# Kernel tuning notes

Hardware: AMD Instinct MI355X
Metric: run time of the kernel (lower is better)

The kernel has to match this reference:

```python
import jax, jax.numpy as jnp
import numpy as np

N0, N1, N2 = 512, 2048, 8192   # targets, hop1, hop2 node counts
K = 33                          # nneighbor + self loop
IN, HID, OUT, NH = 256, 128, 128, 8
NEG = -9.0e15
ALPHA = 0.2                     # LeakyReLU negative slope


def setup_inputs() -> dict:
    key = jax.random.key(0)
    ks = jax.random.split(key, 8)
    feats = jax.random.normal(ks[0], (N2, IN), jnp.float32)
    # xavier-ish scaled params (gain 1.414)
    W1 = jax.random.normal(ks[1], (NH, IN, HID), jnp.float32) * 0.072
    a1 = jax.random.normal(ks[2], (NH, 2 * HID), jnp.float32) * 0.105
    W2 = jax.random.normal(ks[3], (HID * NH, OUT), jnp.float32) * 0.042
    a2 = jax.random.normal(ks[4], (2 * OUT,), jnp.float32) * 0.105
    # layer1 edges: each of N1 targets gets K distinct neighbors in [0, N2)
    tgt1 = jnp.repeat(jnp.arange(N1, dtype=jnp.int32), K)
    dst1 = ((jnp.arange(N1)[:, None] * 97 + jnp.arange(K)[None, :] * 131) % N2).astype(jnp.int32).reshape(-1)
    src1 = jax.random.randint(ks[5], (N1 * K,), 0, N2, jnp.int32)
    # layer2 edges: each of N0 targets gets K distinct neighbors in [0, N1)
    tgt2 = jnp.repeat(jnp.arange(N0, dtype=jnp.int32), K)
    dst2 = ((jnp.arange(N0)[:, None] * 53 + jnp.arange(K)[None, :] * 61) % N1).astype(jnp.int32).reshape(-1)
    src2 = jax.random.randint(ks[6], (N0 * K,), 0, N1, jnp.int32)
    return dict(feats=feats, W1=W1, a1=a1, W2=W2, a2=a2,
                src1=src1, dst1=dst1, tgt1=tgt1, src2=src2, dst2=dst2, tgt2=tgt2)


def gat_layer(x, W, a, src, dst, tgt, t_len):
    # x: [n, in], W: [in, d], a: [2d]
    h = x @ W                                   # [n, d]
    d = h.shape[1]
    # concat([h[src], h[dst]]) @ a  ==  h[src]@a[:d] + h[dst]@a[d:]
    e = h[src] @ a[:d] + h[dst] @ a[d:]         # [E]
    e = jnp.where(e > 0, e, ALPHA * e)          # LeakyReLU
    att = jnp.full((t_len, h.shape[0]), NEG, h.dtype).at[tgt, dst].set(e)
    att = jax.nn.softmax(att, axis=1)           # dense row softmax (masked entries ~0)
    return jax.nn.elu(att @ h)                  # [t_len, d]


def reference(feats, W1, a1, W2, a2, src1, dst1, tgt1, src2, dst2, tgt2):
    # layer 1: nhead independent GAT heads over hop2 features
    heads = jax.vmap(lambda W, a: gat_layer(feats, W, a, src1, dst1, tgt1, N1))(W1, a1)  # [NH, N1, HID]
    x = jnp.transpose(heads, (1, 0, 2)).reshape(N1, NH * HID)  # torch.cat(dim=1)
    # layer 2: single GAT layer producing [N0, OUT]
    return gat_layer(x, W2, a2, src2, dst2, tgt2, N0)
```

## Files before the change

kernel.cpp:

```cpp
#include <hip/hip_runtime.h>
#include <math.h>

#define ALPHA 0.2f

constexpr int CN0 = 512, CN1 = 2048, CN2 = 8192, CK = 33;
constexpr int CIN = 256, CHID = 128, CNH = 8;

using u16    = unsigned short;
using f32x4  = __attribute__((ext_vector_type(4))) float;
using bf16x8 = __attribute__((ext_vector_type(8))) short;
using short8 = __attribute__((ext_vector_type(8))) short;

__device__ __forceinline__ u16 f2bf(float f) {
    unsigned u = __float_as_uint(f);
    u += 0x7fff + ((u >> 16) & 1);
    return (u16)(u >> 16);
}
__device__ __forceinline__ float bf2f(u16 h) {
    return __uint_as_float(((unsigned)h) << 16);
}

#define GLD16(g, l)                                                        \
    __builtin_amdgcn_global_load_lds(                                      \
        (const __attribute__((address_space(1))) void*)(g),                \
        (__attribute__((address_space(3))) void*)(l), 16, 0, 0)

__global__ __launch_bounds__(256) void prep_k(const float* __restrict__ feats,
                                              u16* __restrict__ fb,
                                              const float* __restrict__ W1,
                                              u16* __restrict__ w1t,
                                              const float* __restrict__ W2,
                                              u16* __restrict__ w2t,
                                              const float* __restrict__ a1,
                                              float* __restrict__ pvec) {
    __shared__ float t[32][33];
    int b = blockIdx.x;
    if (b < 2048) {
        const int i = (b * 256 + threadIdx.x) * 4;
        const float4 v = *reinterpret_cast<const float4*>(feats + i);
        *reinterpret_cast<ushort4*>(fb + i) =
            make_ushort4(f2bf(v.x), f2bf(v.y), f2bf(v.z), f2bf(v.w));
        return;
    }
    if (b >= 2432) {
        const int i = b - 2432;
        const int h = i >> 1, half = i & 1;
        const int j = threadIdx.x;
        const float* wrow = W1 + (size_t)h * CIN * CHID + (size_t)j * CHID;
        const float* ah   = a1 + h * 2 * CHID + half * CHID;
        float d = 0.f;
#pragma unroll 8
        for (int c = 0; c < CHID; ++c) d = fmaf(wrow[c], ah[c], d);
        pvec[(h * 2 + half) * CIN + j] = d;
        return;
    }
    b -= 2048;
    const float* ip;
    u16* op;
    int R, C, r0, c0;
    if (b < 256) {
        const int h = b >> 5, w = b & 31;
        ip = W1 + (size_t)h * CIN * CHID;
        op = w1t + (size_t)h * CIN * CHID;
        R = CIN; C = CHID; r0 = (w >> 2) * 32; c0 = (w & 3) * 32;
    } else {
        b -= 256;
        ip = W2; op = w2t;
        R = CNH * CHID; C = CHID; r0 = (b >> 2) * 32; c0 = (b & 3) * 32;
    }
    const int tx = threadIdx.x & 31, ty = threadIdx.x >> 5;
#pragma unroll
    for (int i = 0; i < 4; ++i)
        t[ty + 8 * i][tx] = ip[(size_t)(r0 + ty + 8 * i) * C + c0 + tx];
    __syncthreads();
#pragma unroll
    for (int i = 0; i < 4; ++i)
        op[(size_t)(c0 + ty + 8 * i) * R + r0 + tx] = f2bf(t[tx][ty + 8 * i]);
}

__global__ __launch_bounds__(256) void sgemm1_k(const u16* __restrict__ fb,
                                                const float* __restrict__ pvec,
                                                float* __restrict__ s1,
                                                float* __restrict__ s2) {
    const int node = (blockIdx.x * 256 + threadIdx.x) >> 6;
    const int lane = threadIdx.x & 63;
    const ushort4 hv = *reinterpret_cast<const ushort4*>(fb + (size_t)node * CIN + lane * 4);
    const float v0 = bf2f(hv.x), v1 = bf2f(hv.y), v2 = bf2f(hv.z), v3 = bf2f(hv.w);
#pragma unroll
    for (int h = 0; h < CNH; ++h) {
        const float4 p1 = *reinterpret_cast<const float4*>(pvec + (h * 2 + 0) * CIN + lane * 4);
        const float4 p2 = *reinterpret_cast<const float4*>(pvec + (h * 2 + 1) * CIN + lane * 4);
        float d1 = v0 * p1.x + v1 * p1.y + v2 * p1.z + v3 * p1.w;
        float d2 = v0 * p2.x + v1 * p2.y + v2 * p2.z + v3 * p2.w;
#pragma unroll
        for (int m = 1; m < 64; m <<= 1) {
            d1 += __shfl_xor(d1, m);
            d2 += __shfl_xor(d2, m);
        }
        if (lane == 0) {
            s1[h * CN2 + node] = d1;
            s2[h * CN2 + node] = d2;
        }
    }
}

__global__ __launch_bounds__(128) void agg1g_k(const float* __restrict__ s1,
                                               const float* __restrict__ s2,
                                               const int* __restrict__ src,
                                               const int* __restrict__ dst,
                                               const u16* __restrict__ fb,
                                               u16* __restrict__ gb) {
    __shared__ float wgt[CNH][CK];
    __shared__ int dsts[CK];

    const int t    = blockIdx.x;
    const int tid  = threadIdx.x;
    const int wv   = tid >> 6;
    const int lane = tid & 63;

    int sv = 0, dv = 0;
    if (lane < CK) {
        sv = src[t * CK + lane];
        dv = dst[t * CK + lane];
        if (tid < CK) dsts[tid] = dv;
    }
#pragma unroll
    for (int hh = 0; hh < 4; ++hh) {
        const int head = wv * 4 + hh;
        float e = -3.0e38f;
        if (lane < CK) {
            const float ee = s1[head * CN2 + sv] + s2[head * CN2 + dv];
            e = (ee > 0.f) ? ee : ALPHA * ee;
        }
        float m = e;
#pragma unroll
        for (int mm = 1; mm < 64; mm <<= 1) m = fmaxf(m, __shfl_xor(m, mm));
        const float p = (lane < CK) ? __expf(e - m) : 0.f;
        float s = p;
#pragma unroll
        for (int mm = 1; mm < 64; mm <<= 1) s += __shfl_xor(s, mm);
        if (lane < CK) wgt[head][lane] = p / s;
    }
    __syncthreads();

    const int c2 = tid * 2;
    float acc[CNH][2];
#pragma unroll
    for (int h = 0; h < CNH; ++h) { acc[h][0] = 0.f; acc[h][1] = 0.f; }
#pragma unroll 4
    for (int k = 0; k < CK; ++k) {
        const unsigned w2 = *reinterpret_cast<const unsigned*>(
            fb + (size_t)dsts[k] * CIN + c2);
        const float f0 = bf2f((u16)(w2 & 0xffff));
        const float f1 = bf2f((u16)(w2 >> 16));
#pragma unroll
        for (int h = 0; h < CNH; ++h) {
            const float wk = wgt[h][k];
            acc[h][0] = fmaf(wk, f0, acc[h][0]);
            acc[h][1] = fmaf(wk, f1, acc[h][1]);
        }
    }
#pragma unroll
    for (int h = 0; h < CNH; ++h) {
        const unsigned o = ((unsigned)f2bf(acc[h][1]) << 16) | f2bf(acc[h][0]);
        *reinterpret_cast<unsigned*>(gb + ((size_t)h * CN1 + t) * CIN + c2) = o;
    }
}

template <int KSTEPS, bool BF16OUT, bool ELUOUT, bool HEADSPLIT>
__global__ __launch_bounds__(256) void gemm_mfma(const u16* __restrict__ A, int lda,
                                                 const u16* __restrict__ Bt, int ldb,
                                                 u16* __restrict__ Cb,
                                                 float* __restrict__ Cf, int ldc,
                                                 long csplit) {
    constexpr int SMEMSZ = BF16OUT ? (128 * 136 * 2) : 32768;
    __shared__ __attribute__((aligned(16))) char smem[SMEMSZ];

    const int tid  = threadIdx.x;
    const int lane = tid & 63;
    const int wave = tid >> 6;
    const int row0 = blockIdx.y * 128;

    int kbase, bcol0, ccol0;
    if constexpr (HEADSPLIT) {
        A  += (size_t)blockIdx.z * CN1 * CIN;
        Bt += (size_t)blockIdx.z * CHID * CIN;
        kbase = 0; bcol0 = 0; ccol0 = blockIdx.z * CHID;
    } else {
        kbase = blockIdx.z * (KSTEPS * 32);
        bcol0 = blockIdx.x * 128;
        ccol0 = bcol0;
    }
    const int wr = (wave >> 1) * 64;
    const int wc = (wave & 1) * 64;

    f32x4 acc[4][4];
#pragma unroll
    for (int m = 0; m < 4; ++m)
#pragma unroll
        for (int n = 0; n < 4; ++n) acc[m][n] = (f32x4){0.f, 0.f, 0.f, 0.f};

    const int r0c = tid >> 2;
    const int cs0 = tid & 3;
    const int c0  = (cs0 - (r0c >> 1)) & 3;
    const int r1c = r0c + 64;

    const u16* ga0 = A + (size_t)(row0 + r0c) * lda + kbase + c0 * 8;
    const u16* ga1 = A + (size_t)(row0 + r1c) * lda + kbase + c0 * 8;
    const u16* gb0 = Bt + (size_t)(bcol0 + r0c) * ldb + kbase + c0 * 8;
    const u16* gb1 = Bt + (size_t)(bcol0 + r1c) * ldb + kbase + c0 * 8;

    auto STAGE = [&](int s) {
        const int k0 = s * 32;
        char* base = smem + (s & 1) * 16384;
        u16* as = (u16*)base + wave * 512;
        u16* bs = (u16*)(base + 8192) + wave * 512;
        GLD16(ga0 + k0, as);
        GLD16(ga1 + k0, as + 2048);
        GLD16(gb0 + k0, bs);
        GLD16(gb1 + k0, bs + 2048);
    };

    STAGE(0);
    __syncthreads();

    for (int s = 0; s < KSTEPS; ++s) {
        if (s + 1 < KSTEPS) STAGE(s + 1);

        const u16* Acur = (const u16*)(smem + (s & 1) * 16384);
        const u16* Bcur = Acur + 4096;

        bf16x8 af[4], bfr[4];
#pragma unroll
        for (int m = 0; m < 4; ++m) {
            const int rt = wr + m * 16 + (lane & 15);
            const int cs = ((lane >> 4) + (rt >> 1)) & 3;
            af[m] = *reinterpret_cast<const bf16x8*>(Acur + rt * 32 + cs * 8);
            const int rt2 = wc + m * 16 + (lane & 15);
            const int cs2 = ((lane >> 4) + (rt2 >> 1)) & 3;
            bfr[m] = *reinterpret_cast<const bf16x8*>(Bcur + rt2 * 32 + cs2 * 8);
        }
#pragma unroll
        for (int m = 0; m < 4; ++m)
#pragma unroll
            for (int n = 0; n < 4; ++n)
                acc[m][n] = __builtin_amdgcn_mfma_f32_16x16x32_bf16(
                    af[m], bfr[n], acc[m][n], 0, 0, 0);

        __syncthreads();
    }

    if constexpr (BF16OUT) {
        u16* Cs = (u16*)smem;
#pragma unroll
        for (int m = 0; m < 4; ++m) {
            const int rr = wr + m * 16 + (lane >> 4) * 4;
#pragma unroll
            for (int n = 0; n < 4; ++n) {
                const int cc = wc + n * 16 + (lane & 15);
#pragma unroll
                for (int q = 0; q < 4; ++q) {
                    float v = acc[m][n][q];
                    if (ELUOUT) v = (v > 0.f) ? v : __expf(v) - 1.f;
                    Cs[(rr + q) * 136 + cc] = f2bf(v);
                }
            }
        }
        __syncthreads();
#pragma unroll
        for (int i = 0; i < 8; ++i) {
            const int cid = i * 256 + tid;
            const int r  = cid >> 4;
            const int kc = cid & 15;
            const int4 v = *reinterpret_cast<const int4*>(&Cs[r * 136 + kc * 8]);
            *reinterpret_cast<int4*>(&Cb[(long)(row0 + r) * ldc + ccol0 + kc * 8]) = v;
        }
    } else {
        const long cbase = HEADSPLIT ? 0 : (long)blockIdx.z * csplit;
#pragma unroll
        for (int m = 0; m < 4; ++m) {
            const int rr = row0 + wr + m * 16 + (lane >> 4) * 4;
#pragma unroll
            for (int n = 0; n < 4; ++n) {
                const int cc = ccol0 + wc + n * 16 + (lane & 15);
#pragma unroll
                for (int q = 0; q < 4; ++q)
                    Cf[cbase + (long)(rr + q) * ldc + cc] = acc[m][n][q];
            }
        }
    }
}

__global__ __launch_bounds__(256) void scores2_k(const float* __restrict__ part,
                                                 const float* __restrict__ a,
                                                 float* __restrict__ h2,
                                                 float* __restrict__ s1,
                                                 float* __restrict__ s2) {
    const int wid  = (blockIdx.x * 256 + threadIdx.x) >> 6;
    const int lane = threadIdx.x & 63;
    const int j = lane * 2;
    float x0 = 0.f, x1 = 0.f;
#pragma unroll
    for (int sp = 0; sp < 8; ++sp) {
        const float2 v = *reinterpret_cast<const float2*>(
            part + (size_t)sp * CN1 * CHID + (size_t)wid * CHID + j);
        x0 += v.x; x1 += v.y;
    }
    *reinterpret_cast<float2*>(h2 + (size_t)wid * CHID + j) = make_float2(x0, x1);
    float d1 = x0 * a[j] + x1 * a[j + 1];
    float d2 = x0 * a[CHID + j] + x1 * a[CHID + j + 1];
#pragma unroll
    for (int m = 1; m < 64; m <<= 1) {
        d1 += __shfl_xor(d1, m);
        d2 += __shfl_xor(d2, m);
    }
    if (lane == 0) { s1[wid] = d1; s2[wid] = d2; }
}

__global__ __launch_bounds__(256) void agg2_k(const float* __restrict__ s1,
                                              const float* __restrict__ s2,
                                              const int* __restrict__ src,
                                              const int* __restrict__ dst,
                                              const float* __restrict__ h2,
                                              float* __restrict__ out) {
    const int t    = (blockIdx.x * 256 + threadIdx.x) >> 6;
    const int lane = threadIdx.x & 63;

    float e = -3.0e38f;
    int dv = 0;
    if (lane < CK) {
        const int sv = src[t * CK + lane];
        dv = dst[t * CK + lane];
        const float ee = s1[sv] + s2[dv];
        e = (ee > 0.f) ? ee : ALPHA * ee;
    }
    float m = e;
#pragma unroll
    for (int mm = 1; mm < 64; mm <<= 1) m = fmaxf(m, __shfl_xor(m, mm));
    float p = (lane < CK) ? __expf(e - m) : 0.f;
    float ssum = p;
#pragma unroll
    for (int mm = 1; mm < 64; mm <<= 1) ssum += __shfl_xor(ssum, mm);
    const float invs = 1.f / ssum;

    float a0 = 0.f, a1 = 0.f;
#pragma unroll
    for (int k = 0; k < CK; ++k) {
        const float w = __shfl(p, k) * invs;
        const int d = __shfl(dv, k);
        const float2 hv = *reinterpret_cast<const float2*>(h2 + (size_t)d * CHID + lane * 2);
        a0 = fmaf(w, hv.x, a0);
        a1 = fmaf(w, hv.y, a1);
    }
    a0 = (a0 > 0.f) ? a0 : __expf(a0) - 1.f;
    a1 = (a1 > 0.f) ? a1 : __expf(a1) - 1.f;
    *reinterpret_cast<float2*>(out + (size_t)t * CHID + lane * 2) = make_float2(a0, a1);
}

extern "C" void kernel_launch(void* const* d_in, const int* in_sizes, int n_in,
                              void* d_out, int out_size, void* d_ws, size_t ws_size,
                              hipStream_t stream) {
    const float* feats = (const float*)d_in[0];
    const float* W1    = (const float*)d_in[1];
    const float* a1    = (const float*)d_in[2];
    const float* W2    = (const float*)d_in[3];
    const float* a2    = (const float*)d_in[4];
    const int*   src1  = (const int*)d_in[5];
    const int*   dst1  = (const int*)d_in[6];
    const int*   src2  = (const int*)d_in[8];
    const int*   dst2  = (const int*)d_in[9];
    float* out = (float*)d_out;

    char* w = (char*)d_ws;
    u16*   fb   = (u16*)w;                 w += (size_t)CN2 * CIN * 2;
    u16*   w1t  = (u16*)w;                 w += (size_t)CNH * CIN * CHID * 2;
    u16*   w2t  = (u16*)w;                 w += (size_t)CNH * CHID * CHID * 2;
    float* pvec = (float*)w;               w += (size_t)CNH * 2 * CIN * 4;
    float* s1   = (float*)w;               w += (size_t)CNH * CN2 * 4;
    float* s2   = (float*)w;               w += (size_t)CNH * CN2 * 4;
    u16*   gb   = (u16*)w;                 w += (size_t)CNH * CN1 * CIN * 2;
    u16*   xb   = (u16*)w;                 w += (size_t)CN1 * CNH * CHID * 2;
    float* part = (float*)w;               w += (size_t)8 * CN1 * CHID * 4;
    float* h2   = (float*)w;               w += (size_t)CN1 * CHID * 4;
    float* s21  = (float*)w;               w += (size_t)CN1 * 4;
    float* s22  = (float*)w;               w += (size_t)CN1 * 4;

    prep_k<<<dim3(2048 + 256 + 128 + 16), 256, 0, stream>>>(
        feats, fb, W1, w1t, W2, w2t, a1, pvec);

    sgemm1_k<<<dim3(CN2 / 4), 256, 0, stream>>>(fb, pvec, s1, s2);

    agg1g_k<<<dim3(CN1), 128, 0, stream>>>(s1, s2, src1, dst1, fb, gb);

    gemm_mfma<8, true, true, true><<<dim3(1, CN1 / 128, CNH), 256, 0, stream>>>(
        gb, CIN, w1t, CIN, xb, nullptr, CNH * CHID, 0);

    gemm_mfma<4, false, false, false><<<dim3(1, CN1 / 128, 8), 256, 0, stream>>>(
        xb, CNH * CHID, w2t, CNH * CHID, nullptr, part, CHID, (long)CN1 * CHID);

    scores2_k<<<dim3(CN1 / 4), 256, 0, stream>>>(part, a2, h2, s21, s22);

    agg2_k<<<dim3(CN0 / 4), 256, 0, stream>>>(s21, s22, src2, dst2, h2, out);
}
```

Baseline: 57.74 us.

## Fuse head projection GEMM with layer-2 GEMM and fold feature cast into scoring

```diff
diff --git a/kernel.cpp b/kernel.cpp
--- a/kernel.cpp
+++ b/kernel.cpp
@@ -9,7 +9,6 @@
 using u16    = unsigned short;
 using f32x4  = __attribute__((ext_vector_type(4))) float;
 using bf16x8 = __attribute__((ext_vector_type(8))) short;
-using short8 = __attribute__((ext_vector_type(8))) short;
 
 __device__ __forceinline__ u16 f2bf(float f) {
     unsigned u = __float_as_uint(f);
@@ -25,25 +24,16 @@
         (const __attribute__((address_space(1))) void*)(g),                \
         (__attribute__((address_space(3))) void*)(l), 16, 0, 0)
 
-__global__ __launch_bounds__(256) void prep_k(const float* __restrict__ feats,
-                                              u16* __restrict__ fb,
-                                              const float* __restrict__ W1,
-                                              u16* __restrict__ w1t,
-                                              const float* __restrict__ W2,
-                                              u16* __restrict__ w2t,
-                                              const float* __restrict__ a1,
-                                              float* __restrict__ pvec) {
+__global__ __launch_bounds__(256) void prep2_k(const float* __restrict__ W1,
+                                               u16* __restrict__ w1t,
+                                               const float* __restrict__ W2,
+                                               u16* __restrict__ w2t,
+                                               const float* __restrict__ a1,
+                                               float* __restrict__ pvec) {
     __shared__ float t[32][33];
     int b = blockIdx.x;
-    if (b < 2048) {
-        const int i = (b * 256 + threadIdx.x) * 4;
-        const float4 v = *reinterpret_cast<const float4*>(feats + i);
-        *reinterpret_cast<ushort4*>(fb + i) =
-            make_ushort4(f2bf(v.x), f2bf(v.y), f2bf(v.z), f2bf(v.w));
-        return;
-    }
-    if (b >= 2432) {
-        const int i = b - 2432;
+    if (b >= 384) {
+        const int i = b - 384;
         const int h = i >> 1, half = i & 1;
         const int j = threadIdx.x;
         const float* wrow = W1 + (size_t)h * CIN * CHID + (size_t)j * CHID;
@@ -54,7 +44,6 @@
         pvec[(h * 2 + half) * CIN + j] = d;
         return;
     }
-    b -= 2048;
     const float* ip;
     u16* op;
     int R, C, r0, c0;
@@ -78,20 +67,22 @@
         op[(size_t)(c0 + ty + 8 * i) * R + r0 + tx] = f2bf(t[tx][ty + 8 * i]);
 }
 
-__global__ __launch_bounds__(256) void sgemm1_k(const u16* __restrict__ fb,
-                                                const float* __restrict__ pvec,
-                                                float* __restrict__ s1,
-                                                float* __restrict__ s2) {
+__global__ __launch_bounds__(256) void fsc_k(const float* __restrict__ feats,
+                                             u16* __restrict__ fb,
+                                             const float* __restrict__ pvec,
+                                             float* __restrict__ s1,
+                                             float* __restrict__ s2) {
     const int node = (blockIdx.x * 256 + threadIdx.x) >> 6;
     const int lane = threadIdx.x & 63;
-    const ushort4 hv = *reinterpret_cast<const ushort4*>(fb + (size_t)node * CIN + lane * 4);
-    const float v0 = bf2f(hv.x), v1 = bf2f(hv.y), v2 = bf2f(hv.z), v3 = bf2f(hv.w);
+    const float4 v = *reinterpret_cast<const float4*>(feats + (size_t)node * CIN + lane * 4);
+    *reinterpret_cast<ushort4*>(fb + (size_t)node * CIN + lane * 4) =
+        make_ushort4(f2bf(v.x), f2bf(v.y), f2bf(v.z), f2bf(v.w));
 #pragma unroll
     for (int h = 0; h < CNH; ++h) {
         const float4 p1 = *reinterpret_cast<const float4*>(pvec + (h * 2 + 0) * CIN + lane * 4);
         const float4 p2 = *reinterpret_cast<const float4*>(pvec + (h * 2 + 1) * CIN + lane * 4);
-        float d1 = v0 * p1.x + v1 * p1.y + v2 * p1.z + v3 * p1.w;
-        float d2 = v0 * p2.x + v1 * p2.y + v2 * p2.z + v3 * p2.w;
+        float d1 = v.x * p1.x + v.y * p1.y + v.z * p1.z + v.w * p1.w;
+        float d2 = v.x * p2.x + v.y * p2.y + v.z * p2.z + v.w * p2.w;
 #pragma unroll
         for (int m = 1; m < 64; m <<= 1) {
             d1 += __shfl_xor(d1, m);
@@ -167,36 +158,26 @@
     }
 }
 
-template <int KSTEPS, bool BF16OUT, bool ELUOUT, bool HEADSPLIT>
-__global__ __launch_bounds__(256) void gemm_mfma(const u16* __restrict__ A, int lda,
-                                                 const u16* __restrict__ Bt, int ldb,
-                                                 u16* __restrict__ Cb,
-                                                 float* __restrict__ Cf, int ldc,
-                                                 long csplit) {
-    constexpr int SMEMSZ = BF16OUT ? (128 * 136 * 2) : 32768;
-    __shared__ __attribute__((aligned(16))) char smem[SMEMSZ];
+__global__ __launch_bounds__(256) void fusedproj_k(const u16* __restrict__ gb,
+                                                   const u16* __restrict__ w1t,
+                                                   const u16* __restrict__ w2t,
+                                                   float* __restrict__ part) {
+    __shared__ __attribute__((aligned(16))) char smem[24576];
 
     const int tid  = threadIdx.x;
     const int lane = tid & 63;
     const int wave = tid >> 6;
-    const int row0 = blockIdx.y * 128;
-
-    int kbase, bcol0, ccol0;
-    if constexpr (HEADSPLIT) {
-        A  += (size_t)blockIdx.z * CN1 * CIN;
-        Bt += (size_t)blockIdx.z * CHID * CIN;
-        kbase = 0; bcol0 = 0; ccol0 = blockIdx.z * CHID;
-    } else {
-        kbase = blockIdx.z * (KSTEPS * 32);
-        bcol0 = blockIdx.x * 128;
-        ccol0 = bcol0;
-    }
-    const int wr = (wave >> 1) * 64;
+    const int trow0 = blockIdx.x * 64;
+    const int h     = blockIdx.y;
+    const int wr = (wave >> 1) * 32;
     const int wc = (wave & 1) * 64;
 
-    f32x4 acc[4][4];
-#pragma unroll
-    for (int m = 0; m < 4; ++m)
+    const u16* A  = gb  + (size_t)h * CN1 * CIN;
+    const u16* Bt = w1t + (size_t)h * CHID * CIN;
+
+    f32x4 acc[2][4];
+#pragma unroll
+    for (int m = 0; m < 2; ++m)
 #pragma unroll
         for (int n = 0; n < 4; ++n) acc[m][n] = (f32x4){0.f, 0.f, 0.f, 0.f};
 
@@ -205,18 +186,16 @@
     const int c0  = (cs0 - (r0c >> 1)) & 3;
     const int r1c = r0c + 64;
 
-    const u16* ga0 = A + (size_t)(row0 + r0c) * lda + kbase + c0 * 8;
-    const u16* ga1 = A + (size_t)(row0 + r1c) * lda + kbase + c0 * 8;
-    const u16* gb0 = Bt + (size_t)(bcol0 + r0c) * ldb + kbase + c0 * 8;
-    const u16* gb1 = Bt + (size_t)(bcol0 + r1c) * ldb + kbase + c0 * 8;
+    const u16* ga0 = A + (size_t)(trow0 + r0c) * CIN + c0 * 8;
+    const u16* gb0 = Bt + (size_t)r0c * CIN + c0 * 8;
+    const u16* gb1 = Bt + (size_t)r1c * CIN + c0 * 8;
 
     auto STAGE = [&](int s) {
         const int k0 = s * 32;
-        char* base = smem + (s & 1) * 16384;
+        char* base = smem + (s & 1) * 12288;
         u16* as = (u16*)base + wave * 512;
-        u16* bs = (u16*)(base + 8192) + wave * 512;
+        u16* bs = (u16*)(base + 4096) + wave * 512;
         GLD16(ga0 + k0, as);
-        GLD16(ga1 + k0, as + 2048);
         GLD16(gb0 + k0, bs);
         GLD16(gb1 + k0, bs + 2048);
     };
@@ -224,24 +203,27 @@
     STAGE(0);
     __syncthreads();
 
-    for (int s = 0; s < KSTEPS; ++s) {
-        if (s + 1 < KSTEPS) STAGE(s + 1);
-
-        const u16* Acur = (const u16*)(smem + (s & 1) * 16384);
-        const u16* Bcur = Acur + 4096;
-
-        bf16x8 af[4], bfr[4];
-#pragma unroll
-        for (int m = 0; m < 4; ++m) {
+    for (int s = 0; s < 8; ++s) {
+        if (s + 1 < 8) STAGE(s + 1);
+
+        const u16* Acur = (const u16*)(smem + (s & 1) * 12288);
+        const u16* Bcur = Acur + 2048;
+
+        bf16x8 af[2], bfr[4];
+#pragma unroll
+        for (int m = 0; m < 2; ++m) {
             const int rt = wr + m * 16 + (lane & 15);
             const int cs = ((lane >> 4) + (rt >> 1)) & 3;
             af[m] = *reinterpret_cast<const bf16x8*>(Acur + rt * 32 + cs * 8);
-            const int rt2 = wc + m * 16 + (lane & 15);
+        }
+#pragma unroll
+        for (int n = 0; n < 4; ++n) {
+            const int rt2 = wc + n * 16 + (lane & 15);
             const int cs2 = ((lane >> 4) + (rt2 >> 1)) & 3;
-            bfr[m] = *reinterpret_cast<const bf16x8*>(Bcur + rt2 * 32 + cs2 * 8);
-        }
-#pragma unroll
-        for (int m = 0; m < 4; ++m)
+            bfr[n] = *reinterpret_cast<const bf16x8*>(Bcur + rt2 * 32 + cs2 * 8);
+        }
+#pragma unroll
+        for (int m = 0; m < 2; ++m)
 #pragma unroll
             for (int n = 0; n < 4; ++n)
                 acc[m][n] = __builtin_amdgcn_mfma_f32_16x16x32_bf16(
@@ -250,43 +232,63 @@
         __syncthreads();
     }
 
-    if constexpr (BF16OUT) {
-        u16* Cs = (u16*)smem;
-#pragma unroll
-        for (int m = 0; m < 4; ++m) {
-            const int rr = wr + m * 16 + (lane >> 4) * 4;
-#pragma unroll
-            for (int n = 0; n < 4; ++n) {
-                const int cc = wc + n * 16 + (lane & 15);
-#pragma unroll
-                for (int q = 0; q < 4; ++q) {
-                    float v = acc[m][n][q];
-                    if (ELUOUT) v = (v > 0.f) ? v : __expf(v) - 1.f;
-                    Cs[(rr + q) * 136 + cc] = f2bf(v);
-                }
+    u16* Xs = (u16*)smem;
+#pragma unroll
+    for (int m = 0; m < 2; ++m) {
+        const int rr = wr + m * 16 + (lane >> 4) * 4;
+#pragma unroll
+        for (int n = 0; n < 4; ++n) {
+            const int cc = wc + n * 16 + (lane & 15);
+#pragma unroll
+            for (int q = 0; q < 4; ++q) {
+                float v = acc[m][n][q];
+                v = (v > 0.f) ? v : __expf(v) - 1.f;
+                const int r = rr + q;
+                Xs[r * 128 + ((((cc >> 3) ^ (r & 7)) << 3) | (cc & 7))] = f2bf(v);
             }
         }
-        __syncthreads();
-#pragma unroll
-        for (int i = 0; i < 8; ++i) {
-            const int cid = i * 256 + tid;
-            const int r  = cid >> 4;
-            const int kc = cid & 15;
-            const int4 v = *reinterpret_cast<const int4*>(&Cs[r * 136 + kc * 8]);
-            *reinterpret_cast<int4*>(&Cb[(long)(row0 + r) * ldc + ccol0 + kc * 8]) = v;
-        }
-    } else {
-        const long cbase = HEADSPLIT ? 0 : (long)blockIdx.z * csplit;
-#pragma unroll
-        for (int m = 0; m < 4; ++m) {
-            const int rr = row0 + wr + m * 16 + (lane >> 4) * 4;
-#pragma unroll
-            for (int n = 0; n < 4; ++n) {
-                const int cc = ccol0 + wc + n * 16 + (lane & 15);
-#pragma unroll
-                for (int q = 0; q < 4; ++q)
-                    Cf[cbase + (long)(rr + q) * ldc + cc] = acc[m][n][q];
-            }
+    }
+    __syncthreads();
+
+    f32x4 acc2[2][4];
+#pragma unroll
+    for (int m = 0; m < 2; ++m)
+#pragma unroll
+        for (int n = 0; n < 4; ++n) acc2[m][n] = (f32x4){0.f, 0.f, 0.f, 0.f};
+
+#pragma unroll
+    for (int ks = 0; ks < 4; ++ks) {
+        bf16x8 a2f[2], b2f[4];
+#pragma unroll
+        for (int m = 0; m < 2; ++m) {
+            const int rt = wr + m * 16 + (lane & 15);
+            const int k0 = ks * 32 + (lane >> 4) * 8;
+            a2f[m] = *reinterpret_cast<const bf16x8*>(
+                Xs + rt * 128 + (((k0 >> 3) ^ (rt & 7)) << 3));
+        }
+#pragma unroll
+        for (int n = 0; n < 4; ++n) {
+            const int rb = wc + n * 16 + (lane & 15);
+            b2f[n] = *reinterpret_cast<const bf16x8*>(
+                w2t + (size_t)rb * (CNH * CHID) + h * CHID + ks * 32 + (lane >> 4) * 8);
+        }
+#pragma unroll
+        for (int m = 0; m < 2; ++m)
+#pragma unroll
+            for (int n = 0; n < 4; ++n)
+                acc2[m][n] = __builtin_amdgcn_mfma_f32_16x16x32_bf16(
+                    a2f[m], b2f[n], acc2[m][n], 0, 0, 0);
+    }
+
+#pragma unroll
+    for (int m = 0; m < 2; ++m) {
+        const int rr = trow0 + wr + m * 16 + (lane >> 4) * 4;
+#pragma unroll
+        for (int n = 0; n < 4; ++n) {
+            const int cc = wc + n * 16 + (lane & 15);
+#pragma unroll
+            for (int q = 0; q < 4; ++q)
+                part[((size_t)h * CN1 + rr + q) * CHID + cc] = acc2[m][n][q];
         }
     }
 }
@@ -379,24 +381,18 @@
     float* s1   = (float*)w;               w += (size_t)CNH * CN2 * 4;
     float* s2   = (float*)w;               w += (size_t)CNH * CN2 * 4;
     u16*   gb   = (u16*)w;                 w += (size_t)CNH * CN1 * CIN * 2;
-    u16*   xb   = (u16*)w;                 w += (size_t)CN1 * CNH * CHID * 2;
     float* part = (float*)w;               w += (size_t)8 * CN1 * CHID * 4;
     float* h2   = (float*)w;               w += (size_t)CN1 * CHID * 4;
     float* s21  = (float*)w;               w += (size_t)CN1 * 4;
     float* s22  = (float*)w;               w += (size_t)CN1 * 4;
 
-    prep_k<<<dim3(2048 + 256 + 128 + 16), 256, 0, stream>>>(
-        feats, fb, W1, w1t, W2, w2t, a1, pvec);
-
-    sgemm1_k<<<dim3(CN2 / 4), 256, 0, stream>>>(fb, pvec, s1, s2);
+    prep2_k<<<dim3(256 + 128 + 16), 256, 0, stream>>>(W1, w1t, W2, w2t, a1, pvec);
+
+    fsc_k<<<dim3(CN2 / 4), 256, 0, stream>>>(feats, fb, pvec, s1, s2);
 
     agg1g_k<<<dim3(CN1), 128, 0, stream>>>(s1, s2, src1, dst1, fb, gb);
 
-    gemm_mfma<8, true, true, true><<<dim3(1, CN1 / 128, CNH), 256, 0, stream>>>(
-        gb, CIN, w1t, CIN, xb, nullptr, CNH * CHID, 0);
-
-    gemm_mfma<4, false, false, false><<<dim3(1, CN1 / 128, 8), 256, 0, stream>>>(
-        xb, CNH * CHID, w2t, CNH * CHID, nullptr, part, CHID, (long)CN1 * CHID);
+    fusedproj_k<<<dim3(CN1 / 64, CNH), 256, 0, stream>>>(gb, w1t, w2t, part);
 
     scores2_k<<<dim3(CN1 / 4), 256, 0, stream>>>(part, a2, h2, s21, s22);
 
```

Result: faster. 52.81 us (-8.5%).
